# Performance work log

Measured on AMD Instinct MI355X. Metric: run time of the kernel, lower is better.

Reference implementation:

```python
import jax, jax.numpy as jnp
import numpy as np

B, C, H = 16, 256, 128   # batch, channels (in==out, depthwise), spatial
K, S, P = 3, 2, 1        # kernel, stride, padding (the shape-consistent _Transition config)
LEAVES = 4               # levels=2 -> levels**2


def dwconv(x, w, b, stride, pad):
    # depthwise conv: w is [C,1,K,K] (torch OIHW with groups=C)
    out = jax.lax.conv_general_dilated(
        x, w, (stride, stride), [(pad, pad), (pad, pad)],
        dimension_numbers=('NCHW', 'OIHW', 'NCHW'),
        feature_group_count=x.shape[1])
    return out + b[None, :, None, None]


def maxpool(x, k, s, p):
    # matches nn.MaxPool2d (padding acts as -inf for max)
    return jax.lax.reduce_window(
        x, -jnp.inf, jax.lax.max,
        (1, 1, k, k), (1, 1, s, s),
        [(0, 0), (0, 0), (p, p), (p, p)])


def setup_inputs() -> dict:
    key = jax.random.key(0)
    k0, k1, k2, k3 = jax.random.split(key, 4)
    std = (2.0 / (K * K * C)) ** 0.5  # matches the module's normal_(0, sqrt(2/n)) init
    x = jax.random.normal(k0, (B, C, H, H), jnp.float32)
    maxgate = jax.random.normal(k1, (C, 1, K, K), jnp.float32) * std
    pconvs = jax.random.normal(k2, (C, 1, K, K, LEAVES), jnp.float32) * std  # dw=True
    pgates = jax.random.normal(k3, (C, 1, K, K, 3), jnp.float32) * std       # b=False: (leaves+levels)//2 = 3
    mb = jnp.zeros((C,), jnp.float32)
    pbs = jnp.zeros((C, LEAVES), jnp.float32)
    gbs = jnp.zeros((C, 3), jnp.float32)
    return dict(x=x, maxgate=maxgate, mb=mb, pconvs=pconvs, pbs=pbs,
                pgates=pgates, gbs=gbs)


def reference(x, maxgate, mb, pconvs, pbs, pgates, gbs):
    # max branch: maxpool * depthwise gate conv
    out = maxpool(x, K, S, P) * dwconv(x, maxgate, mb, S, P)

    # leaf stage: 2 sigmoid-gated pool pairs (b=False -> gate2 = 1 - gate1)
    # NOTE: code indexes pgates.select(4, c*2) with gbs.select(1, c)
    leaves = []
    for c in range(LEAVES // 2):
        g1 = jax.nn.sigmoid(dwconv(x, pgates[..., 2 * c], gbs[:, c], S, P))
        p1 = dwconv(x, pconvs[..., 2 * c], pbs[:, 2 * c], S, P)
        p2 = dwconv(x, pconvs[..., 2 * c + 1], pbs[:, 2 * c + 1], S, P)
        leaves.append(g1 * p1)
        leaves.append((1.0 - g1) * p2)

    n0 = leaves[0] + leaves[1]
    n1 = leaves[2] + leaves[3]

    # node stage (kernel_size==3 -> no F.pad); b=False reuses pgates[..., leaves//2 + n] = pgates[...,2]
    g = jax.nn.sigmoid(dwconv(n0, pgates[..., LEAVES // 2], gbs[:, 2], 1, P))
    out = out + n0 * g + n1 * (1.0 - g)
    return out
```

## Files before the change

### kernel.cpp

```cpp
#include <hip/hip_runtime.h>
#include <math.h>

#define TB   512
#define HH   128
#define OHW  64
#define TR   32
#define NT   2
#define XR   69
#define XC   136
#define N0R  34
#define N0C  68

typedef float f32x2 __attribute__((ext_vector_type(2)));

__device__ __forceinline__ float sigmoidf(float z) {
    return 1.0f / (1.0f + __expf(-z));
}

__global__ __launch_bounds__(TB, 8) void fused_densenet_kernel(
    const float* __restrict__ x,
    const float* __restrict__ maxgate,
    const float* __restrict__ mb,
    const float* __restrict__ pconvs,
    const float* __restrict__ pbs,
    const float* __restrict__ pgates,
    const float* __restrict__ gbs,
    float* __restrict__ out)
{
    __shared__ float xs[XR][XC];
    __shared__ float n0s[N0R][N0C];

    const int t     = threadIdx.x;
    const int bid   = blockIdx.x;
    const int tile  = bid & (NT - 1);
    const int plane = bid >> 1;
    const int c     = plane & 255;
    const int r0    = tile * TR;

    float ws[7][9];
#pragma unroll
    for (int i = 0; i < 9; ++i) {
        ws[0][i] = maxgate[c * 9  + i];
        ws[1][i] = pconvs [c * 36 + i * 4 + 0];
        ws[2][i] = pconvs [c * 36 + i * 4 + 1];
        ws[3][i] = pconvs [c * 36 + i * 4 + 2];
        ws[4][i] = pconvs [c * 36 + i * 4 + 3];
        ws[5][i] = pgates [c * 27 + i * 3 + 0];
        ws[6][i] = pgates [c * 27 + i * 3 + 2];
    }
    const float bmax = mb[c];
    const float bp0 = pbs[c * 4 + 0], bp1 = pbs[c * 4 + 1];
    const float bp2 = pbs[c * 4 + 2], bp3 = pbs[c * 4 + 3];
    const float bg0 = gbs[c * 3 + 0];
    const float bg1 = gbs[c * 3 + 1];
    const float bg2 = gbs[c * 3 + 2];

    const float* xplane = x + (size_t)plane * (HH * HH);
    const int ir0 = 2 * r0 - 3;
    for (int s = t; s < XR * 34; s += TB) {
        const int rr = s / 34;
        const int qq = s - rr * 34;
        float4 v = make_float4(0.f, 0.f, 0.f, 0.f);
        const int ir = ir0 + rr;
        if (qq >= 1 && qq <= 32 && (unsigned)ir < (unsigned)HH) {
            v = *reinterpret_cast<const float4*>(xplane + ir * HH + (qq - 1) * 4);
        }
        *reinterpret_cast<float4*>(&xs[rr][qq * 4]) = v;
    }
    __syncthreads();

    if (t < 196) {
        int lrr, li;
        if (t < 66)        { lrr = 0;        li = t + 1;       }
        else if (t < 132)  { lrr = N0R - 1;  li = t - 66 + 1;  }
        else { const int i = t - 132; lrr = 1 + (i >> 1); li = (i & 1) ? 66 : 1; }
        const int gr = r0 - 1 + lrr;
        const int gc = li - 2;
        float n0v = 0.f;
        if ((unsigned)gr < (unsigned)OHW && (unsigned)gc < (unsigned)OHW) {
            float ag = 0.f, a0 = 0.f, a1 = 0.f;
#pragma unroll
            for (int dr = 0; dr < 3; ++dr)
#pragma unroll
                for (int dc = 0; dc < 3; ++dc) {
                    const float v = xs[2 * lrr + dr][2 * gc + dc + 3];
                    const int i = dr * 3 + dc;
                    ag += v * ws[5][i];
                    a0 += v * ws[1][i];
                    a1 += v * ws[2][i];
                }
            const float sg = sigmoidf(ag + bg0);
            n0v = sg * (a0 + bp0) + (1.f - sg) * (a1 + bp1);
        }
        n0s[lrr][li] = n0v;
    }

    const int p  = t & 31;
    const int g0 = t >> 5;
    float out1[2][2], n1v[2][2];

#pragma unroll
    for (int k = 0; k < 2; ++k) {
        const int lr = g0 + 16 * k;
        const int gr = r0 + lr;

        float a[7][2];
#pragma unroll
        for (int ci = 0; ci < 7; ++ci) { a[ci][0] = 0.f; a[ci][1] = 0.f; }
        float mp0 = -INFINITY, mp1 = -INFINITY;

#pragma unroll
        for (int dr = 0; dr < 3; ++dr) {
            const int xr = 2 * lr + 2 + dr;
            const float  v0 = xs[xr][4 * p + 3];
            const float4 vv = *reinterpret_cast<const float4*>(&xs[xr][4 * p + 4]);

            const bool rowok = (gr > 0) | (dr > 0);
            const float h0 = fmaxf(fmaxf((p > 0) ? v0 : -INFINITY, vv.x), vv.y);
            const float h1 = fmaxf(fmaxf(vv.y, vv.z), vv.w);
            mp0 = fmaxf(mp0, rowok ? h0 : -INFINITY);
            mp1 = fmaxf(mp1, rowok ? h1 : -INFINITY);

#pragma unroll
            for (int ci = 0; ci < 7; ++ci) {
                a[ci][0] += v0   * ws[ci][3 * dr] + vv.x * ws[ci][3 * dr + 1] + vv.y * ws[ci][3 * dr + 2];
                a[ci][1] += vv.y * ws[ci][3 * dr] + vv.z * ws[ci][3 * dr + 1] + vv.w * ws[ci][3 * dr + 2];
            }
        }

        const float sg0a = sigmoidf(a[5][0] + bg0);
        const float sg0b = sigmoidf(a[5][1] + bg0);
        const float n0a = sg0a * (a[1][0] + bp0) + (1.f - sg0a) * (a[2][0] + bp1);
        const float n0b = sg0b * (a[1][1] + bp0) + (1.f - sg0b) * (a[2][1] + bp1);
        *reinterpret_cast<f32x2*>(&n0s[lr + 1][2 * p + 2]) = (f32x2){ n0a, n0b };

        const float sg1a = sigmoidf(a[6][0] + bg1);
        const float sg1b = sigmoidf(a[6][1] + bg1);
        n1v[k][0] = sg1a * (a[3][0] + bp2) + (1.f - sg1a) * (a[4][0] + bp3);
        n1v[k][1] = sg1b * (a[3][1] + bp2) + (1.f - sg1b) * (a[4][1] + bp3);
        out1[k][0] = mp0 * (a[0][0] + bmax);
        out1[k][1] = mp1 * (a[0][1] + bmax);
    }
    __syncthreads();

    float* oplane = out + (size_t)plane * (OHW * OHW);
#pragma unroll
    for (int k = 0; k < 2; ++k) {
        const int lr = g0 + 16 * k;
        float ag0 = 0.f, ag1 = 0.f;
        float n0c0 = 0.f, n0c1 = 0.f;
#pragma unroll
        for (int dr = 0; dr < 3; ++dr) {
            const float  e0  = n0s[lr + dr][2 * p + 1];
            const f32x2  mid = *reinterpret_cast<const f32x2*>(&n0s[lr + dr][2 * p + 2]);
            const float  e3  = n0s[lr + dr][2 * p + 4];
            ag0 += e0     * ws[6][3 * dr] + mid.x * ws[6][3 * dr + 1] + mid.y * ws[6][3 * dr + 2];
            ag1 += mid.x  * ws[6][3 * dr] + mid.y * ws[6][3 * dr + 1] + e3    * ws[6][3 * dr + 2];
            if (dr == 1) { n0c0 = mid.x; n0c1 = mid.y; }
        }
        const float ga = sigmoidf(ag0 + bg2);
        const float gb = sigmoidf(ag1 + bg2);
        const float r0v = out1[k][0] + n0c0 * ga + n1v[k][0] * (1.f - ga);
        const float r1v = out1[k][1] + n0c1 * gb + n1v[k][1] * (1.f - gb);
        __builtin_nontemporal_store((f32x2){ r0v, r1v },
            reinterpret_cast<f32x2*>(&oplane[(r0 + lr) * OHW + 2 * p]));
    }
}

extern "C" void kernel_launch(void* const* d_in, const int* in_sizes, int n_in,
                              void* d_out, int out_size, void* d_ws, size_t ws_size,
                              hipStream_t stream) {
    const float* x       = (const float*)d_in[0];
    const float* maxgate = (const float*)d_in[1];
    const float* mb      = (const float*)d_in[2];
    const float* pconvs  = (const float*)d_in[3];
    const float* pbs     = (const float*)d_in[4];
    const float* pgates  = (const float*)d_in[5];
    const float* gbs     = (const float*)d_in[6];
    float* out           = (float*)d_out;

    const int blocks = 16 * 256 * NT;
    fused_densenet_kernel<<<blocks, TB, 0, stream>>>(
        x, maxgate, mb, pconvs, pbs, pgates, gbs, out);
}
```

Measured before the change: 87.02 us.

## Split input tile load in two and overlap second half with first compute pass

The kernel now loads only the first 37 rows of the input tile into shared memory. It issues global loads for the remaining rows into registers and computes the first half of stage 1 while those loads are in flight, then stores them and syncs before the second half. The n0 halo computation is split so the top row is done after the first load and the bottom row after the second, and the side halo columns are simply zeroed. Launch bounds drop from 8 to 6 waves to give room for the extra registers, which reduces occupancy and adds a barrier.

```diff
diff --git a/kernel.cpp b/kernel.cpp
--- a/kernel.cpp
+++ b/kernel.cpp
@@ -10,6 +10,8 @@
 #define XC   136
 #define N0R  34
 #define N0C  68
+#define SLOTS_A (37 * 34)
+#define SLOTS_T (XR * 34)
 
 typedef float f32x2 __attribute__((ext_vector_type(2)));
 
@@ -17,7 +19,7 @@
     return 1.0f / (1.0f + __expf(-z));
 }
 
-__global__ __launch_bounds__(TB, 8) void fused_densenet_kernel(
+__global__ __launch_bounds__(TB, 6) void fused_densenet_kernel(
     const float* __restrict__ x,
     const float* __restrict__ maxgate,
     const float* __restrict__ mb,
@@ -57,7 +59,9 @@
 
     const float* xplane = x + (size_t)plane * (HH * HH);
     const int ir0 = 2 * r0 - 3;
-    for (int s = t; s < XR * 34; s += TB) {
+    float4* xs4 = reinterpret_cast<float4*>(&xs[0][0]);
+
+    for (int s = t; s < SLOTS_A; s += TB) {
         const int rr = s / 34;
         const int qq = s - rr * 34;
         float4 v = make_float4(0.f, 0.f, 0.f, 0.f);
@@ -65,17 +69,32 @@
         if (qq >= 1 && qq <= 32 && (unsigned)ir < (unsigned)HH) {
             v = *reinterpret_cast<const float4*>(xplane + ir * HH + (qq - 1) * 4);
         }
-        *reinterpret_cast<float4*>(&xs[rr][qq * 4]) = v;
-    }
+        xs4[s] = v;
+    }
+    if (t < 2 * N0R) n0s[t >> 1][(t & 1) ? 66 : 1] = 0.f;
     __syncthreads();
 
-    if (t < 196) {
-        int lrr, li;
-        if (t < 66)        { lrr = 0;        li = t + 1;       }
-        else if (t < 132)  { lrr = N0R - 1;  li = t - 66 + 1;  }
-        else { const int i = t - 132; lrr = 1 + (i >> 1); li = (i & 1) ? 66 : 1; }
-        const int gr = r0 - 1 + lrr;
-        const int gc = li - 2;
+    float4 pb[3];
+    int    pbslot[3];
+#pragma unroll
+    for (int j = 0; j < 3; ++j) {
+        const int s = SLOTS_A + t + j * TB;
+        pbslot[j] = (s < SLOTS_T) ? s : -1;
+        float4 v = make_float4(0.f, 0.f, 0.f, 0.f);
+        if (s < SLOTS_T) {
+            const int rr = s / 34;
+            const int qq = s - rr * 34;
+            const int ir = ir0 + rr;
+            if (qq >= 1 && qq <= 32 && ir < HH) {
+                v = *reinterpret_cast<const float4*>(xplane + ir * HH + (qq - 1) * 4);
+            }
+        }
+        pb[j] = v;
+    }
+
+    if (t < 66) {
+        const int gc = t - 1;
+        const int gr = r0 - 1;
         float n0v = 0.f;
         if ((unsigned)gr < (unsigned)OHW && (unsigned)gc < (unsigned)OHW) {
             float ag = 0.f, a0 = 0.f, a1 = 0.f;
@@ -83,7 +102,7 @@
             for (int dr = 0; dr < 3; ++dr)
 #pragma unroll
                 for (int dc = 0; dc < 3; ++dc) {
-                    const float v = xs[2 * lrr + dr][2 * gc + dc + 3];
+                    const float v = xs[dr][2 * gc + dc + 3];
                     const int i = dr * 3 + dc;
                     ag += v * ws[5][i];
                     a0 += v * ws[1][i];
@@ -92,54 +111,80 @@
             const float sg = sigmoidf(ag + bg0);
             n0v = sg * (a0 + bp0) + (1.f - sg) * (a1 + bp1);
         }
-        n0s[lrr][li] = n0v;
+        n0s[0][t + 1] = n0v;
     }
 
     const int p  = t & 31;
     const int g0 = t >> 5;
     float out1[2][2], n1v[2][2];
 
-#pragma unroll
-    for (int k = 0; k < 2; ++k) {
-        const int lr = g0 + 16 * k;
-        const int gr = r0 + lr;
-
-        float a[7][2];
-#pragma unroll
-        for (int ci = 0; ci < 7; ++ci) { a[ci][0] = 0.f; a[ci][1] = 0.f; }
-        float mp0 = -INFINITY, mp1 = -INFINITY;
-
-#pragma unroll
-        for (int dr = 0; dr < 3; ++dr) {
-            const int xr = 2 * lr + 2 + dr;
-            const float  v0 = xs[xr][4 * p + 3];
-            const float4 vv = *reinterpret_cast<const float4*>(&xs[xr][4 * p + 4]);
-
-            const bool rowok = (gr > 0) | (dr > 0);
-            const float h0 = fmaxf(fmaxf((p > 0) ? v0 : -INFINITY, vv.x), vv.y);
-            const float h1 = fmaxf(fmaxf(vv.y, vv.z), vv.w);
-            mp0 = fmaxf(mp0, rowok ? h0 : -INFINITY);
-            mp1 = fmaxf(mp1, rowok ? h1 : -INFINITY);
-
-#pragma unroll
-            for (int ci = 0; ci < 7; ++ci) {
-                a[ci][0] += v0   * ws[ci][3 * dr] + vv.x * ws[ci][3 * dr + 1] + vv.y * ws[ci][3 * dr + 2];
-                a[ci][1] += vv.y * ws[ci][3 * dr] + vv.z * ws[ci][3 * dr + 1] + vv.w * ws[ci][3 * dr + 2];
-            }
-        }
-
-        const float sg0a = sigmoidf(a[5][0] + bg0);
-        const float sg0b = sigmoidf(a[5][1] + bg0);
-        const float n0a = sg0a * (a[1][0] + bp0) + (1.f - sg0a) * (a[2][0] + bp1);
-        const float n0b = sg0b * (a[1][1] + bp0) + (1.f - sg0b) * (a[2][1] + bp1);
-        *reinterpret_cast<f32x2*>(&n0s[lr + 1][2 * p + 2]) = (f32x2){ n0a, n0b };
-
-        const float sg1a = sigmoidf(a[6][0] + bg1);
-        const float sg1b = sigmoidf(a[6][1] + bg1);
-        n1v[k][0] = sg1a * (a[3][0] + bp2) + (1.f - sg1a) * (a[4][0] + bp3);
-        n1v[k][1] = sg1b * (a[3][1] + bp2) + (1.f - sg1b) * (a[4][1] + bp3);
-        out1[k][0] = mp0 * (a[0][0] + bmax);
-        out1[k][1] = mp1 * (a[0][1] + bmax);
+#define STAGE1_BODY(K, LR)                                                              \
+    {                                                                                   \
+        const int lr = (LR);                                                            \
+        const int gr = r0 + lr;                                                         \
+        float a[7][2];                                                                  \
+        _Pragma("unroll")                                                               \
+        for (int ci = 0; ci < 7; ++ci) { a[ci][0] = 0.f; a[ci][1] = 0.f; }              \
+        float mp0 = -INFINITY, mp1 = -INFINITY;                                         \
+        _Pragma("unroll")                                                               \
+        for (int dr = 0; dr < 3; ++dr) {                                                \
+            const int xr = 2 * lr + 2 + dr;                                             \
+            const float  v0 = xs[xr][4 * p + 3];                                        \
+            const float4 vv = *reinterpret_cast<const float4*>(&xs[xr][4 * p + 4]);     \
+            const bool rowok = (gr > 0) | (dr > 0);                                     \
+            const float h0 = fmaxf(fmaxf((p > 0) ? v0 : -INFINITY, vv.x), vv.y);        \
+            const float h1 = fmaxf(fmaxf(vv.y, vv.z), vv.w);                            \
+            mp0 = fmaxf(mp0, rowok ? h0 : -INFINITY);                                   \
+            mp1 = fmaxf(mp1, rowok ? h1 : -INFINITY);                                   \
+            _Pragma("unroll")                                                           \
+            for (int ci = 0; ci < 7; ++ci) {                                            \
+                a[ci][0] += v0   * ws[ci][3*dr] + vv.x * ws[ci][3*dr+1] + vv.y * ws[ci][3*dr+2]; \
+                a[ci][1] += vv.y * ws[ci][3*dr] + vv.z * ws[ci][3*dr+1] + vv.w * ws[ci][3*dr+2]; \
+            }                                                                           \
+        }                                                                               \
+        const float sg0a = sigmoidf(a[5][0] + bg0);                                     \
+        const float sg0b = sigmoidf(a[5][1] + bg0);                                     \
+        const float n0a = sg0a * (a[1][0] + bp0) + (1.f - sg0a) * (a[2][0] + bp1);      \
+        const float n0b = sg0b * (a[1][1] + bp0) + (1.f - sg0b) * (a[2][1] + bp1);      \
+        *reinterpret_cast<f32x2*>(&n0s[lr + 1][2 * p + 2]) = (f32x2){ n0a, n0b };       \
+        const float sg1a = sigmoidf(a[6][0] + bg1);                                     \
+        const float sg1b = sigmoidf(a[6][1] + bg1);                                     \
+        n1v[K][0] = sg1a * (a[3][0] + bp2) + (1.f - sg1a) * (a[4][0] + bp3);            \
+        n1v[K][1] = sg1b * (a[3][1] + bp2) + (1.f - sg1b) * (a[4][1] + bp3);            \
+        out1[K][0] = mp0 * (a[0][0] + bmax);                                            \
+        out1[K][1] = mp1 * (a[0][1] + bmax);                                            \
+    }
+
+    STAGE1_BODY(0, g0)
+
+#pragma unroll
+    for (int j = 0; j < 3; ++j) {
+        if (pbslot[j] >= 0) xs4[pbslot[j]] = pb[j];
+    }
+    __syncthreads();
+
+    STAGE1_BODY(1, g0 + 16)
+
+    if (t < 66) {
+        const int gc = t - 1;
+        const int gr = r0 + TR;
+        float n0v = 0.f;
+        if ((unsigned)gr < (unsigned)OHW && (unsigned)gc < (unsigned)OHW) {
+            float ag = 0.f, a0 = 0.f, a1 = 0.f;
+#pragma unroll
+            for (int dr = 0; dr < 3; ++dr)
+#pragma unroll
+                for (int dc = 0; dc < 3; ++dc) {
+                    const float v = xs[66 + dr][2 * gc + dc + 3];
+                    const int i = dr * 3 + dc;
+                    ag += v * ws[5][i];
+                    a0 += v * ws[1][i];
+                    a1 += v * ws[2][i];
+                }
+            const float sg = sigmoidf(ag + bg0);
+            n0v = sg * (a0 + bp0) + (1.f - sg) * (a1 + bp1);
+        }
+        n0s[N0R - 1][t + 1] = n0v;
     }
     __syncthreads();
 
@@ -165,6 +210,7 @@
         __builtin_nontemporal_store((f32x2){ r0v, r1v },
             reinterpret_cast<f32x2*>(&oplane[(r0 + lr) * OHW + 2 * p]));
     }
+#undef STAGE1_BODY
 }
 
 extern "C" void kernel_launch(void* const* d_in, const int* in_sizes, int n_in,
```

New measurement: 126.3 us. +45.2%, slower.

## Process each plane in one block with double-buffered async global-to-LDS row tiles

Applied to the files above, without the earlier changes.

Each block now handles a whole 128x128 plane as four 16-output-row tiles instead of one of two half-plane tiles per block. Input rows are staged straight into a double-buffered LDS array with global_load_lds, and the next tile is prefetched while the current one is computed. The aim is to hide global load latency behind compute and avoid the register round-trip of the staging copy. In exchange the grid shrinks to 4096 blocks, there are more barriers per block, occupancy falls (launch bounds 6, larger LDS), and the prefetch relies on a hand-written s_waitcnt/s_barrier plus later syncthreads to order the async loads correctly.

```diff
diff --git a/kernel.cpp b/kernel.cpp
--- a/kernel.cpp
+++ b/kernel.cpp
@@ -4,11 +4,9 @@
 #define TB   512
 #define HH   128
 #define OHW  64
-#define TR   32
-#define NT   2
-#define XR   69
-#define XC   136
-#define N0R  34
+#define TR   16
+#define NT   4
+#define XR   37
 #define N0C  68
 
 typedef float f32x2 __attribute__((ext_vector_type(2)));
@@ -17,7 +15,42 @@
     return 1.0f / (1.0f + __expf(-z));
 }
 
-__global__ __launch_bounds__(TB, 8) void fused_densenet_kernel(
+__device__ __forceinline__ void gl2lds16(const float* g, float* l) {
+    __builtin_amdgcn_global_load_lds(
+        (const __attribute__((address_space(1))) void*)g,
+        (__attribute__((address_space(3))) void*)l, 16, 0, 0);
+}
+__device__ __forceinline__ void gl2lds4(const float* g, float* l) {
+    __builtin_amdgcn_global_load_lds(
+        (const __attribute__((address_space(1))) void*)g,
+        (__attribute__((address_space(3))) void*)l, 4, 0, 0);
+}
+
+__device__ __forceinline__ void stage_tile(float* xsbuf, const float* xplane,
+                                           int tt, int t, int wv, int lane) {
+    const int ir0  = 2 * tt * TR - 3;
+    const int lo   = ir0 < 0 ? 0 : ir0;
+    const int hie  = ir0 + XR - 1;
+    const int hi   = hie > HH - 1 ? HH - 1 : hie;
+    const int ztop = lo - ir0;
+    const int zbot = hie - hi;
+    if (ztop && t < ztop * HH) xsbuf[t] = 0.f;
+    if (zbot && t < zbot * HH) xsbuf[(XR - zbot) * HH + t] = 0.f;
+    const int    nfl  = (hi - lo + 1) * HH;
+    const float* gsrc = xplane + lo * HH;
+    float*       ldst = xsbuf + ztop * HH;
+    const int nchunk = nfl >> 8;
+    for (int k = wv; k < nchunk; k += TB / 64) {
+        gl2lds16(gsrc + (k << 8) + lane * 4, ldst + (k << 8));
+    }
+    if ((nfl & 255) && wv == 0) {
+        const int off = nchunk << 8;
+        gl2lds4(gsrc + off + lane,      ldst + off);
+        gl2lds4(gsrc + off + 64 + lane, ldst + off + 64);
+    }
+}
+
+__global__ __launch_bounds__(TB, 6) void fused_densenet_kernel(
     const float* __restrict__ x,
     const float* __restrict__ maxgate,
     const float* __restrict__ mb,
@@ -27,15 +60,16 @@
     const float* __restrict__ gbs,
     float* __restrict__ out)
 {
-    __shared__ float xs[XR][XC];
-    __shared__ float n0s[N0R][N0C];
+    __shared__ float xs[2][XR][HH];
+    __shared__ float n0s[TR + 2][N0C];
 
     const int t     = threadIdx.x;
-    const int bid   = blockIdx.x;
-    const int tile  = bid & (NT - 1);
-    const int plane = bid >> 1;
+    const int lane  = t & 63;
+    const int wv    = t >> 6;
+    const int plane = blockIdx.x;
     const int c     = plane & 255;
-    const int r0    = tile * TR;
+    const int p     = t & 31;
+    const int lr    = t >> 5;
 
     float ws[7][9];
 #pragma unroll
@@ -56,114 +90,96 @@
     const float bg2 = gbs[c * 3 + 2];
 
     const float* xplane = x + (size_t)plane * (HH * HH);
-    const int ir0 = 2 * r0 - 3;
-    for (int s = t; s < XR * 34; s += TB) {
-        const int rr = s / 34;
-        const int qq = s - rr * 34;
-        float4 v = make_float4(0.f, 0.f, 0.f, 0.f);
-        const int ir = ir0 + rr;
-        if (qq >= 1 && qq <= 32 && (unsigned)ir < (unsigned)HH) {
-            v = *reinterpret_cast<const float4*>(xplane + ir * HH + (qq - 1) * 4);
+    float*       op     = out + (size_t)plane * (OHW * OHW);
+
+    stage_tile(&xs[0][0][0], xplane, 0, t, wv, lane);
+    if (t < 2 * (TR + 2)) n0s[t >> 1][(t & 1) ? 66 : 1] = 0.f;
+    __syncthreads();
+
+    for (int tt = 0; tt < NT; ++tt) {
+        const int r0  = tt * TR;
+        const int buf = tt & 1;
+
+        if (tt + 1 < NT) stage_tile(&xs[buf ^ 1][0][0], xplane, tt + 1, t, wv, lane);
+
+        if (t < 132) {
+            const int hb = (t >= 66);
+            const int cc = hb ? t - 66 : t;
+            const int gc = cc - 1;
+            const int gr = hb ? r0 + TR : r0 - 1;
+            float n0v = 0.f;
+            if ((unsigned)gr < (unsigned)OHW && (unsigned)gc < (unsigned)OHW) {
+                float ag = 0.f, a0 = 0.f, a1 = 0.f;
+#pragma unroll
+                for (int dr = 0; dr < 3; ++dr) {
+                    const float* row = xs[buf][(hb ? 2 * TR + 2 : 0) + dr];
+                    const float w0 = (gc > 0) ? row[2 * gc - 1] : 0.f;
+                    const float w1 = row[2 * gc];
+                    const float w2 = row[2 * gc + 1];
+                    ag += w0 * ws[5][3*dr] + w1 * ws[5][3*dr+1] + w2 * ws[5][3*dr+2];
+                    a0 += w0 * ws[1][3*dr] + w1 * ws[1][3*dr+1] + w2 * ws[1][3*dr+2];
+                    a1 += w0 * ws[2][3*dr] + w1 * ws[2][3*dr+1] + w2 * ws[2][3*dr+2];
+                }
+                const float sg = sigmoidf(ag + bg0);
+                n0v = sg * (a0 + bp0) + (1.f - sg) * (a1 + bp1);
+            }
+            n0s[hb ? TR + 1 : 0][cc + 1] = n0v;
         }
-        *reinterpret_cast<float4*>(&xs[rr][qq * 4]) = v;
-    }
-    __syncthreads();
-
-    if (t < 196) {
-        int lrr, li;
-        if (t < 66)        { lrr = 0;        li = t + 1;       }
-        else if (t < 132)  { lrr = N0R - 1;  li = t - 66 + 1;  }
-        else { const int i = t - 132; lrr = 1 + (i >> 1); li = (i & 1) ? 66 : 1; }
-        const int gr = r0 - 1 + lrr;
-        const int gc = li - 2;
-        float n0v = 0.f;
-        if ((unsigned)gr < (unsigned)OHW && (unsigned)gc < (unsigned)OHW) {
-            float ag = 0.f, a0 = 0.f, a1 = 0.f;
-#pragma unroll
-            for (int dr = 0; dr < 3; ++dr)
-#pragma unroll
-                for (int dc = 0; dc < 3; ++dc) {
-                    const float v = xs[2 * lrr + dr][2 * gc + dc + 3];
-                    const int i = dr * 3 + dc;
-                    ag += v * ws[5][i];
-                    a0 += v * ws[1][i];
-                    a1 += v * ws[2][i];
-                }
-            const float sg = sigmoidf(ag + bg0);
-            n0v = sg * (a0 + bp0) + (1.f - sg) * (a1 + bp1);
-        }
-        n0s[lrr][li] = n0v;
-    }
-
-    const int p  = t & 31;
-    const int g0 = t >> 5;
-    float out1[2][2], n1v[2][2];
-
-#pragma unroll
-    for (int k = 0; k < 2; ++k) {
-        const int lr = g0 + 16 * k;
+
         const int gr = r0 + lr;
-
         float a[7][2];
 #pragma unroll
         for (int ci = 0; ci < 7; ++ci) { a[ci][0] = 0.f; a[ci][1] = 0.f; }
         float mp0 = -INFINITY, mp1 = -INFINITY;
-
 #pragma unroll
         for (int dr = 0; dr < 3; ++dr) {
-            const int xr = 2 * lr + 2 + dr;
-            const float  v0 = xs[xr][4 * p + 3];
-            const float4 vv = *reinterpret_cast<const float4*>(&xs[xr][4 * p + 4]);
-
+            const float* row = xs[buf][2 * lr + 2 + dr];
+            const float  v0 = (p > 0) ? row[4 * p - 1] : 0.f;
+            const float4 vv = *reinterpret_cast<const float4*>(&row[4 * p]);
             const bool rowok = (gr > 0) | (dr > 0);
             const float h0 = fmaxf(fmaxf((p > 0) ? v0 : -INFINITY, vv.x), vv.y);
             const float h1 = fmaxf(fmaxf(vv.y, vv.z), vv.w);
             mp0 = fmaxf(mp0, rowok ? h0 : -INFINITY);
             mp1 = fmaxf(mp1, rowok ? h1 : -INFINITY);
-
 #pragma unroll
             for (int ci = 0; ci < 7; ++ci) {
-                a[ci][0] += v0   * ws[ci][3 * dr] + vv.x * ws[ci][3 * dr + 1] + vv.y * ws[ci][3 * dr + 2];
-                a[ci][1] += vv.y * ws[ci][3 * dr] + vv.z * ws[ci][3 * dr + 1] + vv.w * ws[ci][3 * dr + 2];
+                a[ci][0] += v0   * ws[ci][3*dr] + vv.x * ws[ci][3*dr+1] + vv.y * ws[ci][3*dr+2];
+                a[ci][1] += vv.y * ws[ci][3*dr] + vv.z * ws[ci][3*dr+1] + vv.w * ws[ci][3*dr+2];
             }
         }
-
         const float sg0a = sigmoidf(a[5][0] + bg0);
         const float sg0b = sigmoidf(a[5][1] + bg0);
         const float n0a = sg0a * (a[1][0] + bp0) + (1.f - sg0a) * (a[2][0] + bp1);
         const float n0b = sg0b * (a[1][1] + bp0) + (1.f - sg0b) * (a[2][1] + bp1);
         *reinterpret_cast<f32x2*>(&n0s[lr + 1][2 * p + 2]) = (f32x2){ n0a, n0b };
-
         const float sg1a = sigmoidf(a[6][0] + bg1);
         const float sg1b = sigmoidf(a[6][1] + bg1);
-        n1v[k][0] = sg1a * (a[3][0] + bp2) + (1.f - sg1a) * (a[4][0] + bp3);
-        n1v[k][1] = sg1b * (a[3][1] + bp2) + (1.f - sg1b) * (a[4][1] + bp3);
-        out1[k][0] = mp0 * (a[0][0] + bmax);
-        out1[k][1] = mp1 * (a[0][1] + bmax);
-    }
-    __syncthreads();
-
-    float* oplane = out + (size_t)plane * (OHW * OHW);
-#pragma unroll
-    for (int k = 0; k < 2; ++k) {
-        const int lr = g0 + 16 * k;
-        float ag0 = 0.f, ag1 = 0.f;
-        float n0c0 = 0.f, n0c1 = 0.f;
+        const float n1a  = sg1a * (a[3][0] + bp2) + (1.f - sg1a) * (a[4][0] + bp3);
+        const float n1b  = sg1b * (a[3][1] + bp2) + (1.f - sg1b) * (a[4][1] + bp3);
+        const float o1a  = mp0 * (a[0][0] + bmax);
+        const float o1b  = mp1 * (a[0][1] + bmax);
+
+        asm volatile("s_waitcnt lgkmcnt(0)\n\ts_barrier" ::: "memory");
+
+        float ag0 = 0.f, ag1 = 0.f, n0c0 = 0.f, n0c1 = 0.f;
 #pragma unroll
         for (int dr = 0; dr < 3; ++dr) {
-            const float  e0  = n0s[lr + dr][2 * p + 1];
-            const f32x2  mid = *reinterpret_cast<const f32x2*>(&n0s[lr + dr][2 * p + 2]);
-            const float  e3  = n0s[lr + dr][2 * p + 4];
-            ag0 += e0     * ws[6][3 * dr] + mid.x * ws[6][3 * dr + 1] + mid.y * ws[6][3 * dr + 2];
-            ag1 += mid.x  * ws[6][3 * dr] + mid.y * ws[6][3 * dr + 1] + e3    * ws[6][3 * dr + 2];
+            const float e0  = n0s[lr + dr][2 * p + 1];
+            const f32x2 mid = *reinterpret_cast<const f32x2*>(&n0s[lr + dr][2 * p + 2]);
+            const float e3  = n0s[lr + dr][2 * p + 4];
+            ag0 += e0    * ws[6][3*dr] + mid.x * ws[6][3*dr+1] + mid.y * ws[6][3*dr+2];
+            ag1 += mid.x * ws[6][3*dr] + mid.y * ws[6][3*dr+1] + e3    * ws[6][3*dr+2];
             if (dr == 1) { n0c0 = mid.x; n0c1 = mid.y; }
         }
         const float ga = sigmoidf(ag0 + bg2);
         const float gb = sigmoidf(ag1 + bg2);
-        const float r0v = out1[k][0] + n0c0 * ga + n1v[k][0] * (1.f - ga);
-        const float r1v = out1[k][1] + n0c1 * gb + n1v[k][1] * (1.f - gb);
-        __builtin_nontemporal_store((f32x2){ r0v, r1v },
-            reinterpret_cast<f32x2*>(&oplane[(r0 + lr) * OHW + 2 * p]));
+        f32x2 rv;
+        rv.x = o1a + n0c0 * ga + n1a * (1.f - ga);
+        rv.y = o1b + n0c1 * gb + n1b * (1.f - gb);
+        __builtin_nontemporal_store(rv,
+            reinterpret_cast<f32x2*>(op + gr * OHW + 2 * p));
+
+        __syncthreads();
     }
 }
 
@@ -179,7 +195,7 @@
     const float* gbs     = (const float*)d_in[6];
     float* out           = (float*)d_out;
 
-    const int blocks = 16 * 256 * NT;
+    const int blocks = 16 * 256;
     fused_densenet_kernel<<<blocks, TB, 0, stream>>>(
         x, maxgate, mb, pconvs, pbs, pgates, gbs, out);
 }
```

Result: slower. 100.9 us (+16.0%).
